# Kernel optimization log

Measured on AMD Instinct MI355X. Metric: run time of the kernel, lower is better.

## Reference

```python
import jax, jax.numpy as jnp
import numpy as np

N, D, R, OUT, B = 4096, 128, 8, 128, 4096

def setup_inputs() -> dict:
    key = jax.random.key(0)
    ks = jax.random.split(key, 8)
    return {
        "embeddings": jax.random.normal(ks[0], (N, D), dtype=jnp.float32),
        "head_idx": jax.random.randint(ks[1], (B,), 0, N),
        "head_e": jax.random.normal(ks[2], (B, D), dtype=jnp.float32),
        "tail_idx": jax.random.randint(ks[3], (B,), 0, N),
        "tail_e": jax.random.normal(ks[4], (B, D), dtype=jnp.float32),
        "adj_mats": jax.random.uniform(ks[5], (R, N, N), dtype=jnp.float32),
        "relation_kernel": jax.random.normal(ks[6], (R, D, OUT), dtype=jnp.float32),
        "self_kernel": jax.random.normal(ks[7], (D, OUT), dtype=jnp.float32),
    }

def _branch(idx, e, adj_mats, embeddings, relation_kernel, self_kernel):
    # self transform: [B, OUT]
    out = e @ self_kernel
    # per-relation row gather: [R, B, N]
    adj = adj_mats[:, idx, :]
    # neighborhood aggregation: [R, B, D]
    upd = jnp.einsum('rbn,nd->rbd', adj, embeddings)
    # relation transform + accumulate over relations: [B, OUT]
    out = out + jnp.einsum('rbd,rdo->bo', upd, relation_kernel)
    return out

def reference(embeddings, head_idx, head_e, tail_idx, tail_e, adj_mats, relation_kernel, self_kernel):
    head_output = _branch(head_idx, head_e, adj_mats, embeddings, relation_kernel, self_kernel)
    tail_output = _branch(tail_idx, tail_e, adj_mats, embeddings, relation_kernel, self_kernel)
    return (head_output, tail_output)
```

## Files before the change

### kernel.cpp

```cpp
#include <hip/hip_runtime.h>

#define NN   4096
#define DD   128
#define RR   8
#define OUTD 128
#define BB   4096

typedef unsigned short ushort_t;
typedef __attribute__((ext_vector_type(8))) short short8;
typedef __attribute__((ext_vector_type(4))) float floatx4;

__device__ __forceinline__ ushort_t f2bf(float f) {
  union { float f; unsigned int u; } v; v.f = f;
  unsigned int u = v.u;
  return (ushort_t)((u + 0x7fffu + ((u >> 16) & 1u)) >> 16);
}

__device__ __forceinline__ unsigned int pk2(float x, float y) {
  union { float f; unsigned int u; } a, b;
  a.f = x; b.f = y;
  const unsigned int ua = a.u + 0x8000u;
  const unsigned int ub = b.u + 0x8000u;
  return __builtin_amdgcn_perm(ub, ua, 0x07060302u);
}

__device__ __forceinline__ short8 pack8(float4 a, float4 b) {
  union { unsigned int u[4]; short8 s; } r;
  r.u[0] = pk2(a.x, a.y); r.u[1] = pk2(a.z, a.w);
  r.u[2] = pk2(b.x, b.y); r.u[3] = pk2(b.z, b.w);
  return r.s;
}

__global__ __launch_bounds__(256) void compute_wt(const float* __restrict__ emb,
                                                  const float* __restrict__ rk,
                                                  ushort_t* __restrict__ Wt) {
  __shared__ float e_s[64][132];
  __shared__ float k_s[128][36];
  const int r  = blockIdx.y;
  const int m0 = blockIdx.x * 64;
  const int t  = threadIdx.x;
  {
    const int row = t >> 2, q = t & 3;
    const float* src = emb + (size_t)(m0 + row) * DD;
    #pragma unroll
    for (int j = 0; j < 8; ++j) {
      const int c = q + 4 * j;
      *(float4*)&e_s[row][c * 4] = *(const float4*)(src + c * 4);
    }
  }
  const int m_l = t >> 2, ob = (t & 3) * 8;
  const float* rkr = rk + (size_t)r * DD * OUTD;
  #pragma unroll 1
  for (int oc = 0; oc < 4; ++oc) {
    __syncthreads();
    {
      const int d = t >> 1, h = (t & 1) * 4;
      #pragma unroll
      for (int j = 0; j < 4; ++j) {
        const int c = h + j;
        *(float4*)&k_s[d][c * 4] = *(const float4*)(rkr + d * OUTD + oc * 32 + c * 4);
      }
    }
    __syncthreads();
    float acc[8] = {0, 0, 0, 0, 0, 0, 0, 0};
    #pragma unroll 4
    for (int d = 0; d < DD; ++d) {
      const float e  = e_s[m_l][d];
      const float4 w0 = *(const float4*)&k_s[d][ob];
      const float4 w1 = *(const float4*)&k_s[d][ob + 4];
      acc[0] += e * w0.x; acc[1] += e * w0.y; acc[2] += e * w0.z; acc[3] += e * w0.w;
      acc[4] += e * w1.x; acc[5] += e * w1.y; acc[6] += e * w1.z; acc[7] += e * w1.w;
    }
    ushort_t* dst = Wt + ((size_t)r * OUTD + oc * 32 + ob) * NN + m0 + m_l;
    #pragma unroll
    for (int j = 0; j < 8; ++j) dst[(size_t)j * NN] = f2bf(acc[j]);
  }
}

__global__ __launch_bounds__(256) void rgcn_main(const float* __restrict__ adj,
                                                 const ushort_t* __restrict__ Wt,
                                                 float* __restrict__ Z) {
  __shared__ short8 A8[1024];
  __shared__ short8 B8[2048];
  const int r     = blockIdx.y >> 1;
  const int khalf = (blockIdx.y & 1) * 2048;
  const int n0    = blockIdx.x * 64;
  const int t = threadIdx.x;
  const int lane = t & 63, wave = t >> 6;
  const int wm = wave >> 1, wn = wave & 1;
  const int l15 = lane & 15, l4 = lane >> 4;
  const float*    adjr = adj + (size_t)r * NN * NN + (size_t)n0 * NN;
  const ushort_t* wtr  = Wt + (size_t)r * OUTD * NN;

  floatx4 acc[2][4] = {};

  const int arow = t >> 2, aq = t & 3;

  for (int k0 = khalf; k0 < khalf + 2048; k0 += 128) {
    const float4* asrc = (const float4*)(adjr + (size_t)arow * NN + k0) + aq * 8;
    float4 av[8];
    #pragma unroll
    for (int j = 0; j < 8; ++j) av[j] = asrc[j];
    #pragma unroll
    for (int it = 0; it < 8; ++it) {
      const int s = wave * 512 + it * 64 + lane;
      const int o = s >> 4, kc = s & 15;
      const int gkc = kc ^ (o & 15);
      const ushort_t* gp = wtr + (size_t)o * NN + k0 + gkc * 8;
      __builtin_amdgcn_global_load_lds(
          (const __attribute__((address_space(1))) void*)gp,
          (__attribute__((address_space(3))) void*)&B8[wave * 512 + it * 64],
          16, 0, 0);
    }
    #pragma unroll
    for (int j = 0; j < 4; ++j) {
      const int ck = aq * 4 + j;
      A8[arow * 16 + (ck ^ (arow & 15))] = pack8(av[2 * j], av[2 * j + 1]);
    }
    __syncthreads();
    #pragma unroll
    for (int kk = 0; kk < 4; ++kk) {
      short8 af[2], bf[4];
      #pragma unroll
      for (int ti = 0; ti < 2; ++ti) {
        const int row = wm * 32 + ti * 16 + l15;
        af[ti] = A8[row * 16 + ((kk * 4 + l4) ^ (row & 15))];
      }
      #pragma unroll
      for (int tj = 0; tj < 4; ++tj) {
        const int orow = wn * 64 + tj * 16 + l15;
        bf[tj] = B8[orow * 16 + ((kk * 4 + l4) ^ (orow & 15))];
      }
      #pragma unroll
      for (int ti = 0; ti < 2; ++ti)
        #pragma unroll
        for (int tj = 0; tj < 4; ++tj)
          acc[ti][tj] = __builtin_amdgcn_mfma_f32_16x16x32_bf16(af[ti], bf[tj],
                                                                acc[ti][tj], 0, 0, 0);
    }
    __syncthreads();
  }
  #pragma unroll
  for (int ti = 0; ti < 2; ++ti)
    #pragma unroll
    for (int tj = 0; tj < 4; ++tj)
      #pragma unroll
      for (int j = 0; j < 4; ++j) {
        const int nrow = n0 + wm * 32 + ti * 16 + l4 * 4 + j;
        const int ocol = wn * 64 + tj * 16 + l15;
        atomicAdd(Z + (size_t)nrow * OUTD + ocol, acc[ti][tj][j]);
      }
}

__global__ __launch_bounds__(256) void epilogue_k(const float* __restrict__ he,
                                                  const float* __restrict__ te,
                                                  const int* __restrict__ hidx,
                                                  const int* __restrict__ tidx,
                                                  const float* __restrict__ sk,
                                                  const float* __restrict__ Z,
                                                  float* __restrict__ out) {
  __shared__ float e_s[64][132];
  __shared__ float k_s[128][36];
  const int bx = blockIdx.x;
  const int branch = bx >> 6;
  const int row0 = (bx & 63) * 64;
  const float* e  = branch ? te : he;
  const int* idx  = branch ? tidx : hidx;
  float* ob = out + (size_t)branch * BB * OUTD;
  const int t = threadIdx.x;
  {
    const int row = t >> 2, q = t & 3;
    const float* src = e + (size_t)(row0 + row) * DD;
    #pragma unroll
    for (int j = 0; j < 8; ++j) {
      const int c = q + 4 * j;
      *(float4*)&e_s[row][c * 4] = *(const float4*)(src + c * 4);
    }
  }
  const int m_l = t >> 2, obk = (t & 3) * 8;
  const int zi = idx[row0 + m_l];
  const float* zrow = Z + (size_t)zi * OUTD;
  #pragma unroll 1
  for (int oc = 0; oc < 4; ++oc) {
    __syncthreads();
    {
      const int d = t >> 1, h = (t & 1) * 4;
      #pragma unroll
      for (int j = 0; j < 4; ++j) {
        const int c = h + j;
        *(float4*)&k_s[d][c * 4] = *(const float4*)(sk + d * OUTD + oc * 32 + c * 4);
      }
    }
    __syncthreads();
    float acc[8] = {0, 0, 0, 0, 0, 0, 0, 0};
    #pragma unroll 4
    for (int d = 0; d < DD; ++d) {
      const float ev = e_s[m_l][d];
      const float4 w0 = *(const float4*)&k_s[d][obk];
      const float4 w1 = *(const float4*)&k_s[d][obk + 4];
      acc[0] += ev * w0.x; acc[1] += ev * w0.y; acc[2] += ev * w0.z; acc[3] += ev * w0.w;
      acc[4] += ev * w1.x; acc[5] += ev * w1.y; acc[6] += ev * w1.z; acc[7] += ev * w1.w;
    }
    const float4 z0 = *(const float4*)(zrow + oc * 32 + obk);
    const float4 z1 = *(const float4*)(zrow + oc * 32 + obk + 4);
    float4 o0, o1;
    o0.x = acc[0] + z0.x; o0.y = acc[1] + z0.y; o0.z = acc[2] + z0.z; o0.w = acc[3] + z0.w;
    o1.x = acc[4] + z1.x; o1.y = acc[5] + z1.y; o1.z = acc[6] + z1.z; o1.w = acc[7] + z1.w;
    *(float4*)&ob[(size_t)(row0 + m_l) * OUTD + oc * 32 + obk]     = o0;
    *(float4*)&ob[(size_t)(row0 + m_l) * OUTD + oc * 32 + obk + 4] = o1;
  }
}

extern "C" void kernel_launch(void* const* d_in, const int* in_sizes, int n_in,
                              void* d_out, int out_size, void* d_ws, size_t ws_size,
                              hipStream_t stream) {
  const float* emb  = (const float*)d_in[0];
  const int*   hidx = (const int*)  d_in[1];
  const float* he   = (const float*)d_in[2];
  const int*   tidx = (const int*)  d_in[3];
  const float* te   = (const float*)d_in[4];
  const float* adj  = (const float*)d_in[5];
  const float* rk   = (const float*)d_in[6];
  const float* sk   = (const float*)d_in[7];
  float* out = (float*)d_out;

  ushort_t* Wt = (ushort_t*)d_ws;
  float*    Z  = (float*)((char*)d_ws + (size_t)RR * OUTD * NN * sizeof(ushort_t));

  hipMemsetAsync(Z, 0, (size_t)NN * OUTD * sizeof(float), stream);
  compute_wt<<<dim3(64, 8), 256, 0, stream>>>(emb, rk, Wt);
  rgcn_main<<<dim3(64, 16), 256, 0, stream>>>(adj, Wt, Z);
  epilogue_k<<<dim3(128), 256, 0, stream>>>(he, te, hidx, tidx, sk, Z, out);
}
```

Measured before the change: 754.6 us.

## Double-buffer B tiles, feed A fragments from registers, drop atomics for per-relation partials

The main GEMM kernel now handles the full K range per relation. It double-buffers the Wt tile in LDS so the next tile's async load overlaps the current MFMA work. The adjacency operand is read with nontemporal loads directly into per-lane MFMA fragments, which removes the A staging in LDS and one barrier per iteration. Atomic accumulation into a single Z is replaced by plain stores into per-relation partial buffers that the epilogue sums, so the memset goes away. In exchange the grid is halved, which reduces parallelism, and workspace use grows by 8x for Z.

```diff
diff --git a/kernel.cpp b/kernel.cpp
--- a/kernel.cpp
+++ b/kernel.cpp
@@ -24,10 +24,10 @@
   return __builtin_amdgcn_perm(ub, ua, 0x07060302u);
 }
 
-__device__ __forceinline__ short8 pack8(float4 a, float4 b) {
+__device__ __forceinline__ short8 pack8(floatx4 a, floatx4 b) {
   union { unsigned int u[4]; short8 s; } r;
-  r.u[0] = pk2(a.x, a.y); r.u[1] = pk2(a.z, a.w);
-  r.u[2] = pk2(b.x, b.y); r.u[3] = pk2(b.z, b.w);
+  r.u[0] = pk2(a[0], a[1]); r.u[1] = pk2(a[2], a[3]);
+  r.u[2] = pk2(b[0], b[1]); r.u[3] = pk2(b[2], b[3]);
   return r.s;
 }
 
@@ -77,30 +77,24 @@
   }
 }
 
-__global__ __launch_bounds__(256) void rgcn_main(const float* __restrict__ adj,
-                                                 const ushort_t* __restrict__ Wt,
-                                                 float* __restrict__ Z) {
-  __shared__ short8 A8[1024];
-  __shared__ short8 B8[2048];
-  const int r     = blockIdx.y >> 1;
-  const int khalf = (blockIdx.y & 1) * 2048;
-  const int n0    = blockIdx.x * 64;
+__global__ __launch_bounds__(256, 2) void rgcn_main(const float* __restrict__ adj,
+                                                    const ushort_t* __restrict__ Wt,
+                                                    float* __restrict__ Zr) {
+  __shared__ short8 B8[2][2048];
+  const int r  = blockIdx.y;
+  const int n0 = blockIdx.x * 64;
   const int t = threadIdx.x;
   const int lane = t & 63, wave = t >> 6;
-  const int wm = wave >> 1, wn = wave & 1;
   const int l15 = lane & 15, l4 = lane >> 4;
-  const float*    adjr = adj + (size_t)r * NN * NN + (size_t)n0 * NN;
-  const ushort_t* wtr  = Wt + (size_t)r * OUTD * NN;
-
-  floatx4 acc[2][4] = {};
-
-  const int arow = t >> 2, aq = t & 3;
-
-  for (int k0 = khalf; k0 < khalf + 2048; k0 += 128) {
-    const float4* asrc = (const float4*)(adjr + (size_t)arow * NN + k0) + aq * 8;
-    float4 av[8];
-    #pragma unroll
-    for (int j = 0; j < 8; ++j) av[j] = asrc[j];
+  const float* __restrict__ arow =
+      adj + (size_t)r * NN * NN + (size_t)(n0 + wave * 16 + l15) * NN;
+  const ushort_t* __restrict__ wtr = Wt + (size_t)r * OUTD * NN;
+
+  floatx4 acc[8] = {};
+  floatx4 av[8];
+  short8  af[4];
+
+  auto stageB = [&](int buf, int k0) {
     #pragma unroll
     for (int it = 0; it < 8; ++it) {
       const int s = wave * 512 + it * 64 + lane;
@@ -109,47 +103,53 @@
       const ushort_t* gp = wtr + (size_t)o * NN + k0 + gkc * 8;
       __builtin_amdgcn_global_load_lds(
           (const __attribute__((address_space(1))) void*)gp,
-          (__attribute__((address_space(3))) void*)&B8[wave * 512 + it * 64],
+          (__attribute__((address_space(3))) void*)&B8[buf][wave * 512 + it * 64],
           16, 0, 0);
     }
-    #pragma unroll
-    for (int j = 0; j < 4; ++j) {
-      const int ck = aq * 4 + j;
-      A8[arow * 16 + (ck ^ (arow & 15))] = pack8(av[2 * j], av[2 * j + 1]);
-    }
-    __syncthreads();
+  };
+  auto loadA = [&](int k0) {
     #pragma unroll
     for (int kk = 0; kk < 4; ++kk) {
-      short8 af[2], bf[4];
-      #pragma unroll
-      for (int ti = 0; ti < 2; ++ti) {
-        const int row = wm * 32 + ti * 16 + l15;
-        af[ti] = A8[row * 16 + ((kk * 4 + l4) ^ (row & 15))];
+      const floatx4* p = (const floatx4*)(arow + k0 + kk * 32 + l4 * 8);
+      av[2 * kk]     = __builtin_nontemporal_load(p);
+      av[2 * kk + 1] = __builtin_nontemporal_load(p + 1);
+    }
+  };
+
+  stageB(0, 0);
+  loadA(0);
+  __syncthreads();
+
+  int cur = 0;
+  #pragma unroll 1
+  for (int kt = 0; kt < 32; ++kt) {
+    if (kt + 1 < 32) stageB(cur ^ 1, (kt + 1) * 128);
+    #pragma unroll
+    for (int kk = 0; kk < 4; ++kk) af[kk] = pack8(av[2 * kk], av[2 * kk + 1]);
+    if (kt + 1 < 32) loadA((kt + 1) * 128);
+    #pragma unroll
+    for (int kk = 0; kk < 4; ++kk) {
+      short8 bf[8];
+      #pragma unroll
+      for (int tj = 0; tj < 8; ++tj) {
+        const int orow = tj * 16 + l15;
+        bf[tj] = B8[cur][orow * 16 + ((kk * 4 + l4) ^ (orow & 15))];
       }
       #pragma unroll
-      for (int tj = 0; tj < 4; ++tj) {
-        const int orow = wn * 64 + tj * 16 + l15;
-        bf[tj] = B8[orow * 16 + ((kk * 4 + l4) ^ (orow & 15))];
-      }
-      #pragma unroll
-      for (int ti = 0; ti < 2; ++ti)
-        #pragma unroll
-        for (int tj = 0; tj < 4; ++tj)
-          acc[ti][tj] = __builtin_amdgcn_mfma_f32_16x16x32_bf16(af[ti], bf[tj],
-                                                                acc[ti][tj], 0, 0, 0);
-    }
-    __syncthreads();
-  }
+      for (int tj = 0; tj < 8; ++tj)
+        acc[tj] = __builtin_amdgcn_mfma_f32_16x16x32_bf16(af[kk], bf[tj],
+                                                          acc[tj], 0, 0, 0);
+    }
+    __syncthreads();
+    cur ^= 1;
+  }
+
+  float* zout = Zr + ((size_t)r * NN + n0 + wave * 16) * OUTD;
   #pragma unroll
-  for (int ti = 0; ti < 2; ++ti)
-    #pragma unroll
-    for (int tj = 0; tj < 4; ++tj)
-      #pragma unroll
-      for (int j = 0; j < 4; ++j) {
-        const int nrow = n0 + wm * 32 + ti * 16 + l4 * 4 + j;
-        const int ocol = wn * 64 + tj * 16 + l15;
-        atomicAdd(Z + (size_t)nrow * OUTD + ocol, acc[ti][tj][j]);
-      }
+  for (int tj = 0; tj < 8; ++tj)
+    #pragma unroll
+    for (int j = 0; j < 4; ++j)
+      zout[(size_t)(l4 * 4 + j) * OUTD + tj * 16 + l15] = acc[tj][j];
 }
 
 __global__ __launch_bounds__(256) void epilogue_k(const float* __restrict__ he,
@@ -157,7 +157,7 @@
                                                   const int* __restrict__ hidx,
                                                   const int* __restrict__ tidx,
                                                   const float* __restrict__ sk,
-                                                  const float* __restrict__ Z,
+                                                  const float* __restrict__ Zr,
                                                   float* __restrict__ out) {
   __shared__ float e_s[64][132];
   __shared__ float k_s[128][36];
@@ -179,7 +179,6 @@
   }
   const int m_l = t >> 2, obk = (t & 3) * 8;
   const int zi = idx[row0 + m_l];
-  const float* zrow = Z + (size_t)zi * OUTD;
   #pragma unroll 1
   for (int oc = 0; oc < 4; ++oc) {
     __syncthreads();
@@ -201,13 +200,20 @@
       acc[0] += ev * w0.x; acc[1] += ev * w0.y; acc[2] += ev * w0.z; acc[3] += ev * w0.w;
       acc[4] += ev * w1.x; acc[5] += ev * w1.y; acc[6] += ev * w1.z; acc[7] += ev * w1.w;
     }
-    const float4 z0 = *(const float4*)(zrow + oc * 32 + obk);
-    const float4 z1 = *(const float4*)(zrow + oc * 32 + obk + 4);
-    float4 o0, o1;
-    o0.x = acc[0] + z0.x; o0.y = acc[1] + z0.y; o0.z = acc[2] + z0.z; o0.w = acc[3] + z0.w;
-    o1.x = acc[4] + z1.x; o1.y = acc[5] + z1.y; o1.z = acc[6] + z1.z; o1.w = acc[7] + z1.w;
-    *(float4*)&ob[(size_t)(row0 + m_l) * OUTD + oc * 32 + obk]     = o0;
-    *(float4*)&ob[(size_t)(row0 + m_l) * OUTD + oc * 32 + obk + 4] = o1;
+    floatx4 z0 = {0.f, 0.f, 0.f, 0.f}, z1 = {0.f, 0.f, 0.f, 0.f};
+    #pragma unroll
+    for (int rr = 0; rr < RR; ++rr) {
+      const float* zrow = Zr + ((size_t)rr * NN + zi) * OUTD + oc * 32;
+      z0 += *(const floatx4*)(zrow + obk);
+      z1 += *(const floatx4*)(zrow + obk + 4);
+    }
+    floatx4 o0, o1;
+    o0[0] = acc[0] + z0[0]; o0[1] = acc[1] + z0[1];
+    o0[2] = acc[2] + z0[2]; o0[3] = acc[3] + z0[3];
+    o1[0] = acc[4] + z1[0]; o1[1] = acc[5] + z1[1];
+    o1[2] = acc[6] + z1[2]; o1[3] = acc[7] + z1[3];
+    *(floatx4*)&ob[(size_t)(row0 + m_l) * OUTD + oc * 32 + obk]     = o0;
+    *(floatx4*)&ob[(size_t)(row0 + m_l) * OUTD + oc * 32 + obk + 4] = o1;
   }
 }
 
@@ -225,10 +231,9 @@
   float* out = (float*)d_out;
 
   ushort_t* Wt = (ushort_t*)d_ws;
-  float*    Z  = (float*)((char*)d_ws + (size_t)RR * OUTD * NN * sizeof(ushort_t));
-
-  hipMemsetAsync(Z, 0, (size_t)NN * OUTD * sizeof(float), stream);
+  float*    Zr = (float*)((char*)d_ws + (size_t)RR * OUTD * NN * sizeof(ushort_t));
+
   compute_wt<<<dim3(64, 8), 256, 0, stream>>>(emb, rk, Wt);
-  rgcn_main<<<dim3(64, 16), 256, 0, stream>>>(adj, Wt, Z);
-  epilogue_k<<<dim3(128), 256, 0, stream>>>(he, te, hidx, tidx, sk, Z, out);
-}
+  rgcn_main<<<dim3(64, 8), 256, 0, stream>>>(adj, Wt, Zr);
+  epilogue_k<<<dim3(128), 256, 0, stream>>>(he, te, hidx, tidx, sk, Zr, out);
+}
```

Result: no change. 750.1 us (median of 2 runs) (-0.6%).
